# Kernel tuning notes

Hardware: AMD Instinct MI355X
Metric: run time of the kernel (lower is better)

## Reference

```python
import jax, jax.numpy as jnp
import numpy as np

B, S, D = 4, 4096, 1024

def setup_inputs() -> dict:
    key = jax.random.key(0)
    kx, kq, kk, kv = jax.random.split(key, 4)
    x = jax.random.normal(kx, (B, S, D), dtype=jnp.float32)
    # nn.Linear weights, stored here as [d_in, d_out] so y = x @ W
    scale = 1.0 / np.sqrt(D)
    Wq = jax.random.normal(kq, (D, D), dtype=jnp.float32) * scale
    Wk = jax.random.normal(kk, (D, D), dtype=jnp.float32) * scale
    Wv = jax.random.normal(kv, (D, D), dtype=jnp.float32) * scale
    return {"x": x, "Wq": Wq, "Wk": Wk, "Wv": Wv}

def reference(x, Wq, Wk, Wv):
    b, n, d_in = x.shape
    d_out = Wk.shape[1]
    q = jnp.einsum('bnd,de->bne', x, Wq)
    k = jnp.einsum('bnd,de,->bne', x, Wk, 1.0)  # keys
    v = jnp.einsum('bnd,de->bne', x, Wv)
    # full causal attention: scores scaled by 1/sqrt(d_out) AFTER masking (matches source)
    scores = jnp.einsum('bqe,bke->bqk', q, k)
    causal = jnp.triu(jnp.ones((n, n), dtype=bool), k=1)  # True above diagonal -> masked
    scores = jnp.where(causal[None, :, :], -jnp.inf, scores)
    attn = jax.nn.softmax(scores / jnp.sqrt(jnp.asarray(d_out, scores.dtype)), axis=-1)
    # dropout p=0.0 (eval) -> identity
    return jnp.einsum('bqk,bke->bqe', attn, v)
```

## Files before the change

kernel.cpp:

```cpp
#include <hip/hip_runtime.h>
#include <hip/hip_bf16.h>

#define B_ 4
#define S_ 4096
#define D_ 1024
#define NT_ 32
#define PAIRS_ 528

typedef __attribute__((ext_vector_type(8))) short short8;
typedef __attribute__((ext_vector_type(4))) float f32x4;

__device__ __forceinline__ unsigned short f2bf(float f) {
    union { float f; unsigned u; } v; v.f = f;
    unsigned u = v.u;
    return (unsigned short)((u + 0x7fffu + ((u >> 16) & 1u)) >> 16);
}

__device__ __forceinline__ void gld_lds16(const unsigned short* g, unsigned short* l) {
    __builtin_amdgcn_global_load_lds((const __attribute__((address_space(1))) void*)g,
                                     (__attribute__((address_space(3))) void*)l, 16, 0, 0);
}

__device__ __forceinline__ void stage128x32(const unsigned short* gbase, size_t ld,
                                            unsigned short* ls, int tid) {
    const int r = tid >> 2;
    const int c = (tid & 3) * 8;
    unsigned short* lw = ls + tid * 8;
    gld_lds16(gbase + (size_t)r * ld + c, lw);
    gld_lds16(gbase + (size_t)(r + 64) * ld + c, lw + 2048);
}

__global__ __launch_bounds__(256) void prep_x(const float* __restrict__ x,
                                              unsigned short* __restrict__ xb) {
    size_t i = ((size_t)blockIdx.x * 256 + threadIdx.x) * 8;
    float4 a = *(const float4*)&x[i];
    float4 b = *(const float4*)&x[i + 4];
    unsigned u0 = (unsigned)f2bf(a.x) | ((unsigned)f2bf(a.y) << 16);
    unsigned u1 = (unsigned)f2bf(a.z) | ((unsigned)f2bf(a.w) << 16);
    unsigned u2 = (unsigned)f2bf(b.x) | ((unsigned)f2bf(b.y) << 16);
    unsigned u3 = (unsigned)f2bf(b.z) | ((unsigned)f2bf(b.w) << 16);
    uint4 val; val.x = u0; val.y = u1; val.z = u2; val.w = u3;
    *(uint4*)&xb[i] = val;
}

__global__ __launch_bounds__(256) void prep_w(const float* __restrict__ Wq,
                                              const float* __restrict__ Wk,
                                              const float* __restrict__ Wv,
                                              unsigned short* __restrict__ Wt) {
    __shared__ float ls[64 * 65];
    const int z = blockIdx.z;
    const float* __restrict__ W = (z == 0) ? Wq : (z == 1) ? Wk : Wv;
    unsigned short* __restrict__ Wtz = Wt + (size_t)z * D_ * D_;
    const int k0 = blockIdx.y * 64, n0 = blockIdx.x * 64;
    const int tid = threadIdx.x;
    #pragma unroll
    for (int i = 0; i < 16; ++i) {
        int lin = i * 256 + tid, r = lin >> 6, c = lin & 63;
        ls[r * 65 + c] = W[(size_t)(k0 + r) * D_ + n0 + c];
    }
    __syncthreads();
    #pragma unroll
    for (int i = 0; i < 16; ++i) {
        int lin = i * 256 + tid, r = lin >> 6, c = lin & 63;
        Wtz[(size_t)(n0 + r) * D_ + k0 + c] = f2bf(ls[c * 65 + r]);
    }
}

__global__ __launch_bounds__(512, 2) void qkv_gemm(
    const unsigned short* __restrict__ xb, const unsigned short* __restrict__ Wt,
    unsigned short* __restrict__ Q, unsigned short* __restrict__ K,
    unsigned short* __restrict__ V)
{
    __shared__ __align__(16) unsigned short lsA[2 * 256 * 64];
    __shared__ __align__(16) unsigned short lsB[2 * 256 * 64];

    const int z = blockIdx.z;
    unsigned short* __restrict__ Y = (z == 0) ? Q : (z == 1) ? K : V;
    const float scale = (z == 0) ? 0.03125f : 1.0f;

    const int lin = blockIdx.x;
    const int wg = (lin & 7) * 32 + (lin >> 3);
    const int m0 = (wg >> 2) * 256, n0 = (wg & 3) * 256;

    const int tid = threadIdx.x, lane = tid & 63, w = tid >> 6;
    const int wm = w >> 2, wn = w & 3;
    const int quad = lane >> 4, ln = lane & 15;

    const unsigned short* Ab = xb + (size_t)m0 * D_;
    const unsigned short* Bb = Wt + (size_t)z * D_ * D_ + (size_t)n0 * D_;

#define STAGE_HALF(gbase, ldsbase)                                              \
    {                                                                           \
        _Pragma("unroll")                                                       \
        for (int i_ = 0; i_ < 2; ++i_) {                                        \
            int g_ = tid + i_ * 512;                                            \
            int r_ = g_ >> 3;                                                   \
            int cg_ = (g_ & 7) ^ (r_ & 7);                                      \
            gld_lds16((gbase) + (size_t)r_ * D_ + cg_ * 8, (ldsbase) + g_ * 8); \
        }                                                                       \
    }
#define STAGE(kt, h)                                                                   \
    {                                                                                  \
        if ((h) < 2) { STAGE_HALF(Ab + (size_t)((h) * 128) * D_ + (kt) * 64,           \
                                  &lsA[(((kt) & 1) * 2 + (h)) * 8192]) }               \
        else         { STAGE_HALF(Bb + (size_t)(((h) - 2) * 128) * D_ + (kt) * 64,     \
                                  &lsB[(((kt) & 1) * 2 + ((h) - 2)) * 8192]) }         \
    }

    const unsigned short* As;
    const unsigned short* Bs;
    short8 a[4][2], b[2][2];
    f32x4 acc[8][4] = {};

#define LDA(mh)                                                                        \
    {                                                                                  \
        _Pragma("unroll")                                                              \
        for (int mf_ = 0; mf_ < 4; ++mf_) {                                            \
            _Pragma("unroll")                                                          \
            for (int ks_ = 0; ks_ < 2; ++ks_) {                                        \
                int r_ = wm * 128 + ((mh) * 4 + mf_) * 16 + ln;                        \
                int cg_ = ks_ * 4 + quad;                                              \
                a[mf_][ks_] = *(const short8*)&As[r_ * 64 + ((cg_ ^ (r_ & 7)) << 3)];  \
            }                                                                          \
        }                                                                              \
    }
#define LDB(nh)                                                                        \
    {                                                                                  \
        _Pragma("unroll")                                                              \
        for (int nf_ = 0; nf_ < 2; ++nf_) {                                            \
            _Pragma("unroll")                                                          \
            for (int ks_ = 0; ks_ < 2; ++ks_) {                                        \
                int r_ = wn * 64 + ((nh) * 2 + nf_) * 16 + ln;                         \
                int cg_ = ks_ * 4 + quad;                                              \
                b[nf_][ks_] = *(const short8*)&Bs[r_ * 64 + ((cg_ ^ (r_ & 7)) << 3)];  \
            }                                                                          \
        }                                                                              \
    }
#define MM(mh, nh)                                                                     \
    {                                                                                  \
        __builtin_amdgcn_s_setprio(1);                                                 \
        _Pragma("unroll")                                                              \
        for (int mf_ = 0; mf_ < 4; ++mf_)                                              \
            _Pragma("unroll")                                                          \
            for (int nf_ = 0; nf_ < 2; ++nf_)                                          \
                _Pragma("unroll")                                                      \
                for (int ks_ = 0; ks_ < 2; ++ks_)                                      \
                    acc[(mh) * 4 + mf_][(nh) * 2 + nf_] =                              \
                        __builtin_amdgcn_mfma_f32_16x16x32_bf16(                       \
                            a[mf_][ks_], b[nf_][ks_],                                  \
                            acc[(mh) * 4 + mf_][(nh) * 2 + nf_], 0, 0, 0);             \
        __builtin_amdgcn_s_setprio(0);                                                 \
    }
#define LGKM0 asm volatile("s_waitcnt lgkmcnt(0)" ::: "memory")
#define BAR   __builtin_amdgcn_s_barrier()

    STAGE(0, 0) STAGE(0, 1) STAGE(0, 2) STAGE(0, 3)
    STAGE(1, 0) STAGE(1, 1)
    asm volatile("s_waitcnt vmcnt(4)" ::: "memory");
    BAR;

    #pragma unroll 2
    for (int t = 0; t < 16; ++t) {
        As = lsA + (t & 1) * 16384;
        Bs = lsB + (t & 1) * 16384;
        LDA(0) LDB(0)
        if (t < 15) STAGE(t + 1, 2)
        BAR; LGKM0;
        MM(0, 0)
        BAR;
        LDB(1)
        if (t < 15) STAGE(t + 1, 3)
        BAR; LGKM0;
        MM(0, 1)
        BAR;
        LDA(1)
        BAR; LGKM0;
        MM(1, 1)
        BAR;
        LDB(0)
        if (t < 14) { STAGE(t + 2, 0) STAGE(t + 2, 1) }
        BAR; LGKM0;
        MM(1, 0)
        if (t < 14)       asm volatile("s_waitcnt vmcnt(4)" ::: "memory");
        else if (t == 14) asm volatile("s_waitcnt vmcnt(0)" ::: "memory");
        if (t < 15) BAR;
    }

#undef STAGE_HALF
#undef STAGE
#undef LDA
#undef LDB
#undef MM
#undef LGKM0
#undef BAR

    #pragma unroll
    for (int mf = 0; mf < 8; ++mf)
        #pragma unroll
        for (int nf = 0; nf < 4; ++nf)
            #pragma unroll
            for (int rr = 0; rr < 4; ++rr) {
                int row = m0 + wm * 128 + mf * 16 + quad * 4 + rr;
                int col = n0 + wn * 64 + nf * 16 + ln;
                Y[(size_t)row * D_ + col] = f2bf(acc[mf][nf][rr] * scale);
            }
}

__global__ __launch_bounds__(256) void vt_trans(const unsigned short* __restrict__ V,
                                                unsigned short* __restrict__ Vt) {
    __shared__ unsigned short ls[64 * 66];
    const int s0 = blockIdx.x * 64, e0 = blockIdx.y * 64, b = blockIdx.z;
    const int tid = threadIdx.x;
    const size_t base = (size_t)b * S_ * D_;
    #pragma unroll
    for (int i = 0; i < 16; ++i) {
        int lin = i * 256 + tid, r = lin >> 6, c = lin & 63;
        ls[r * 66 + c] = V[base + (size_t)(s0 + r) * D_ + e0 + c];
    }
    __syncthreads();
    const size_t baseT = (size_t)b * D_ * S_;
    #pragma unroll
    for (int i = 0; i < 16; ++i) {
        int lin = i * 256 + tid, r = lin >> 6, c = lin & 63;
        Vt[baseT + (size_t)(e0 + r) * S_ + s0 + c] = ls[c * 66 + r];
    }
}

__global__ __launch_bounds__(256) void qk_pexp(
    const unsigned short* __restrict__ Q, const unsigned short* __restrict__ K,
    unsigned short* __restrict__ P, float* __restrict__ lpart)
{
    __shared__ __align__(16) unsigned short lsA[4096];
    __shared__ __align__(16) unsigned short lsB[4096];
    __shared__ float sml[2][128];

    const int l = blockIdx.x, b = blockIdx.y;
    const int r = l & 7;
    const int s = l >> 3;
    int qt, kt;
    if (s < r + 1)            { qt = r;      kt = s; }
    else if (s < 33)          { qt = 31 - r; kt = s - (r + 1); }
    else if (s < 42 + r)      { qt = 8 + r;  kt = s - 33; }
    else                      { qt = 23 - r; kt = s - (42 + r); }
    const int p = qt * (qt + 1) / 2 + kt;

    const int q0 = qt * 128, k0 = kt * 128;
    const int tid = threadIdx.x, lane = tid & 63, w = tid >> 6;
    const int wm = w >> 1, wn = w & 1, quad = lane >> 4, ln = lane & 15;
    const size_t base = (size_t)b * S_ * D_;

    const unsigned short* Qb = Q + base + (size_t)q0 * D_;
    const unsigned short* Kb = K + base + (size_t)k0 * D_;

    f32x4 acc[4][4] = {};
    for (int et = 0; et < D_ / 32; ++et) {
        stage128x32(Qb + et * 32, D_, lsA, tid);
        stage128x32(Kb + et * 32, D_, lsB, tid);
        __syncthreads();
        short8 af[4], bfr[4];
        #pragma unroll
        for (int mf = 0; mf < 4; ++mf)
            af[mf] = *(const short8*)&lsA[(wm * 64 + mf * 16 + ln) * 32 + quad * 8];
        #pragma unroll
        for (int nf = 0; nf < 4; ++nf)
            bfr[nf] = *(const short8*)&lsB[(wn * 64 + nf * 16 + ln) * 32 + quad * 8];
        #pragma unroll
        for (int mf = 0; mf < 4; ++mf)
            #pragma unroll
            for (int nf = 0; nf < 4; ++nf)
                acc[mf][nf] = __builtin_amdgcn_mfma_f32_16x16x32_bf16(af[mf], bfr[nf], acc[mf][nf], 0, 0, 0);
        __syncthreads();
    }

    const bool diag = (kt == qt);
    unsigned short* Pt = P + ((size_t)b * PAIRS_ + p) * (128 * 128);

    #pragma unroll
    for (int mf = 0; mf < 4; ++mf)
        #pragma unroll
        for (int rr = 0; rr < 4; ++rr) {
            int rowq = wm * 64 + mf * 16 + quad * 4 + rr;
            float lsum = 0.0f;
            #pragma unroll
            for (int nf = 0; nf < 4; ++nf) {
                int ckey = wn * 64 + nf * 16 + ln;
                float sc = acc[mf][nf][rr];
                float pe = (diag && ckey > rowq) ? 0.0f : __expf(fminf(sc, 60.0f));
                Pt[rowq * 128 + ckey] = f2bf(pe);
                lsum += pe;
            }
            #pragma unroll
            for (int off = 1; off < 16; off <<= 1)
                lsum += __shfl_xor(lsum, off);
            if (ln == 0) sml[wn][rowq] = lsum;
        }
    __syncthreads();

    if (tid < 128)
        lpart[((size_t)b * PAIRS_ + p) * 128 + tid] = sml[0][tid] + sml[1][tid];
}

__global__ __launch_bounds__(128) void merge_il(const float* __restrict__ lpart,
                                                float* __restrict__ il) {
    const int qt = blockIdx.x, b = blockIdx.y;
    const int row = threadIdx.x;
    const int pbase = qt * (qt + 1) / 2;
    float l = 0.0f;
    for (int kt = 0; kt <= qt; ++kt)
        l += lpart[((size_t)b * PAIRS_ + pbase + kt) * 128 + row];
    il[(size_t)b * S_ + qt * 128 + row] = 1.0f / l;
}

__global__ __launch_bounds__(256) void pv_gemm(
    const unsigned short* __restrict__ P, const unsigned short* __restrict__ Vt,
    const float* __restrict__ il, float* __restrict__ O)
{
    __shared__ __align__(16) unsigned short lsA[4096];
    __shared__ __align__(16) unsigned short lsB[4096];

    const int l = blockIdx.x;
    const int dt = l & 7;
    const int s = l >> 3;
    const int pair = s & 15;
    const int b = s >> 4;
    const int d0 = dt * 128;
    const int tid = threadIdx.x, lane = tid & 63, w = tid >> 6;
    const int wm = w >> 1, wn = w & 1, quad = lane >> 4, ln = lane & 15;

    const unsigned short* Vtb = Vt + ((size_t)b * D_ + d0) * S_;

    #pragma unroll 1
    for (int half = 0; half < 2; ++half) {
        const int qt = half ? pair : (31 - pair);
        const int q0 = qt * 128;
        const int pbase = qt * (qt + 1) / 2;

        f32x4 acc[4][4] = {};

        #pragma unroll 1
        for (int ktile = 0; ktile <= qt; ++ktile) {
            const unsigned short* Ptile = P + ((size_t)b * PAIRS_ + pbase + ktile) * (128 * 128);
            #pragma unroll 1
            for (int sub = 0; sub < 4; ++sub) {
                stage128x32(Ptile + sub * 32, 128, lsA, tid);
                stage128x32(Vtb + ktile * 128 + sub * 32, S_, lsB, tid);
                __syncthreads();
                short8 af[4], bfr[4];
                #pragma unroll
                for (int mf = 0; mf < 4; ++mf)
                    af[mf] = *(const short8*)&lsA[(wm * 64 + mf * 16 + ln) * 32 + quad * 8];
                #pragma unroll
                for (int nf = 0; nf < 4; ++nf)
                    bfr[nf] = *(const short8*)&lsB[(wn * 64 + nf * 16 + ln) * 32 + quad * 8];
                #pragma unroll
                for (int mf = 0; mf < 4; ++mf)
                    #pragma unroll
                    for (int nf = 0; nf < 4; ++nf)
                        acc[mf][nf] = __builtin_amdgcn_mfma_f32_16x16x32_bf16(af[mf], bfr[nf], acc[mf][nf], 0, 0, 0);
                __syncthreads();
            }
        }

        #pragma unroll
        for (int mf = 0; mf < 4; ++mf) {
            float ilv[4];
            #pragma unroll
            for (int rr = 0; rr < 4; ++rr)
                ilv[rr] = il[(size_t)b * S_ + q0 + wm * 64 + mf * 16 + quad * 4 + rr];
            #pragma unroll
            for (int nf = 0; nf < 2; ++nf)
                #pragma unroll
                for (int rr = 0; rr < 4; ++rr) {
                    int rowq = q0 + wm * 64 + mf * 16 + quad * 4 + rr;
                    int col = d0 + wn * 64 + nf * 16 + ln;
                    O[((size_t)b * S_ + rowq) * D_ + col] = acc[mf][nf][rr] * ilv[rr];
                }
            #pragma unroll
            for (int nf = 2; nf < 4; ++nf)
                #pragma unroll
                for (int rr = 0; rr < 4; ++rr) {
                    int rowq = q0 + wm * 64 + mf * 16 + quad * 4 + rr;
                    int col = d0 + wn * 64 + nf * 16 + ln;
                    O[((size_t)b * S_ + rowq) * D_ + col] = acc[mf][nf][rr] * ilv[rr];
                }
        }
    }
}

extern "C" void kernel_launch(void* const* d_in, const int* in_sizes, int n_in,
                              void* d_out, int out_size, void* d_ws, size_t ws_size,
                              hipStream_t stream) {
    const float* x  = (const float*)d_in[0];
    const float* Wq = (const float*)d_in[1];
    const float* Wk = (const float*)d_in[2];
    const float* Wv = (const float*)d_in[3];

    const size_t nQ = (size_t)B_ * S_ * D_;
    const size_t nP = (size_t)B_ * PAIRS_ * 128 * 128;

    unsigned short* P  = (unsigned short*)d_ws;
    unsigned short* V  = P;
    unsigned short* Q  = P + nP;
    unsigned short* K  = Q + nQ;
    unsigned short* Vt = K + nQ;
    unsigned short* xb = Vt;
    unsigned short* Wt = Vt + nQ;
    float* lpart = (float*)(Wt + (size_t)3 * D_ * D_);
    float* il    = lpart + (size_t)B_ * PAIRS_ * 128;
    float* O = (float*)d_out;

    hipLaunchKernelGGL(prep_x, dim3(8192), dim3(256), 0, stream, x, xb);
    hipLaunchKernelGGL(prep_w, dim3(16, 16, 3), dim3(256), 0, stream, Wq, Wk, Wv, Wt);
    hipLaunchKernelGGL(qkv_gemm, dim3(256, 1, 3), dim3(512), 0, stream, xb, Wt, Q, K, V);
    hipLaunchKernelGGL(vt_trans, dim3(64, 16, B_), dim3(256), 0, stream, V, Vt);
    hipLaunchKernelGGL(qk_pexp, dim3(PAIRS_, B_), dim3(256), 0, stream, Q, K, P, lpart);
    hipLaunchKernelGGL(merge_il, dim3(NT_, B_), dim3(128), 0, stream, lpart, il);
    hipLaunchKernelGGL(pv_gemm, dim3(512), dim3(256), 0, stream, P, Vt, il, O);
}
```

Before: 457.9 us.

## Simplify projection GEMM pipeline to whole-tile prefetch with one barrier per step

The projection GEMM main loop now issues all four staging loads for the next K-tile at the top of each iteration. It then runs the four quadrant MFMA phases back-to-back with no intermediate barriers or LDS waits, and ends with a single vmcnt(0) wait and one barrier per step. The previous schedule interleaved half-tile staging with four barrier-separated phases and prefetched partly two tiles ahead. The aim is to cut barrier and wait overhead and let the compiler schedule LDS reads and MFMAs more freely. The cost is a shallower prefetch, since a full vmcnt(0) drain now happens every iteration. A duplicated epilogue loop is also merged, which is cosmetic.

```diff
diff --git a/kernel.cpp b/kernel.cpp
--- a/kernel.cpp
+++ b/kernel.cpp
@@ -152,38 +152,33 @@
         __builtin_amdgcn_s_setprio(0);                                                 \
     }
 #define LGKM0 asm volatile("s_waitcnt lgkmcnt(0)" ::: "memory")
+#define VM0   asm volatile("s_waitcnt vmcnt(0)" ::: "memory")
 #define BAR   __builtin_amdgcn_s_barrier()
+#define SB0   __builtin_amdgcn_sched_barrier(0)
 
     STAGE(0, 0) STAGE(0, 1) STAGE(0, 2) STAGE(0, 3)
-    STAGE(1, 0) STAGE(1, 1)
-    asm volatile("s_waitcnt vmcnt(4)" ::: "memory");
-    BAR;
+    VM0; SB0;
+    BAR; SB0;
 
     #pragma unroll 2
     for (int t = 0; t < 16; ++t) {
         As = lsA + (t & 1) * 16384;
         Bs = lsB + (t & 1) * 16384;
+        if (t < 15) { STAGE(t + 1, 0) STAGE(t + 1, 1) STAGE(t + 1, 2) STAGE(t + 1, 3) }
+        SB0;
         LDA(0) LDB(0)
-        if (t < 15) STAGE(t + 1, 2)
-        BAR; LGKM0;
         MM(0, 0)
-        BAR;
         LDB(1)
-        if (t < 15) STAGE(t + 1, 3)
-        BAR; LGKM0;
         MM(0, 1)
-        BAR;
         LDA(1)
-        BAR; LGKM0;
         MM(1, 1)
-        BAR;
         LDB(0)
-        if (t < 14) { STAGE(t + 2, 0) STAGE(t + 2, 1) }
-        BAR; LGKM0;
         MM(1, 0)
-        if (t < 14)       asm volatile("s_waitcnt vmcnt(4)" ::: "memory");
-        else if (t == 14) asm volatile("s_waitcnt vmcnt(0)" ::: "memory");
-        if (t < 15) BAR;
+        LGKM0; SB0;
+        if (t < 15) {
+            VM0; SB0;
+            BAR; SB0;
+        }
     }
 
 #undef STAGE_HALF
@@ -192,7 +187,9 @@
 #undef LDB
 #undef MM
 #undef LGKM0
+#undef VM0
 #undef BAR
+#undef SB0
 
     #pragma unroll
     for (int mf = 0; mf < 8; ++mf)
@@ -368,15 +365,7 @@
             for (int rr = 0; rr < 4; ++rr)
                 ilv[rr] = il[(size_t)b * S_ + q0 + wm * 64 + mf * 16 + quad * 4 + rr];
             #pragma unroll
-            for (int nf = 0; nf < 2; ++nf)
-                #pragma unroll
-                for (int rr = 0; rr < 4; ++rr) {
-                    int rowq = q0 + wm * 64 + mf * 16 + quad * 4 + rr;
-                    int col = d0 + wn * 64 + nf * 16 + ln;
-                    O[((size_t)b * S_ + rowq) * D_ + col] = acc[mf][nf][rr] * ilv[rr];
-                }
-            #pragma unroll
-            for (int nf = 2; nf < 4; ++nf)
+            for (int nf = 0; nf < 4; ++nf)
                 #pragma unroll
                 for (int rr = 0; rr < 4; ++rr) {
                     int rowq = q0 + wm * 64 + mf * 16 + quad * 4 + rr;
```

Result: faster. 442.1 us (-3.4%).
